# Kernel tuning notes

Measured on AMD Instinct MI355X. Metric: run time of the kernel, lower is better.

The kernel has to match this reference:

```python
import jax, jax.numpy as jnp
import numpy as np

B, C, N, K, OUT = 4, 3, 32768, 16, 64


def setup_inputs() -> dict:
    key = jax.random.key(0)
    k1, k2, k3, k4, k5, k6 = jax.random.split(key, 6)
    coords = jax.random.normal(k1, (B, C, N), dtype=jnp.float32)
    knn_indices = jax.random.randint(k2, (B, N, K), 0, N, dtype=jnp.int64)
    # Conv2d(3, 64, (1,1)) weight is (out, in, 1, 1) -> store as (out, in)
    W1 = jax.random.normal(k3, (OUT, C), dtype=jnp.float32) * (1.0 / np.sqrt(C))
    b1 = jax.random.normal(k4, (OUT,), dtype=jnp.float32) * 0.01
    W2 = jax.random.normal(k5, (OUT, OUT), dtype=jnp.float32) * (1.0 / np.sqrt(OUT))
    b2 = jax.random.normal(k6, (OUT,), dtype=jnp.float32) * 0.01
    return {"coords": coords, "knn_indices": knn_indices,
            "W1": W1, "b1": b1, "W2": W2, "b2": b2}


def reference(coords, knn_indices, W1, b1, W2, b2):
    b, c, n = coords.shape
    _, _, k = knn_indices.shape
    # index2points: gather neighbor coords -> (B, C, N, K)
    idx = knn_indices.reshape(b, 1, n * k)                      # (B,1,N*K)
    idx = jnp.broadcast_to(idx, (b, c, n * k))
    knn_coords = jnp.take_along_axis(coords, idx, axis=2).reshape(b, c, n, k)
    # localize(coords, knn_coords) * -1  ==  coords - knn_coords
    coords_space = coords[:, :, :, None] - knn_coords           # (B,C,N,K)
    # 1x1 conv MLP: conv -> relu -> conv
    h = jnp.einsum('oc,bcnk->bonk', W1, coords_space) + b1[None, :, None, None]
    h = jax.nn.relu(h)
    out = jnp.einsum('oc,bcnk->bonk', W2, h) + b2[None, :, None, None]
    return out
```

## Files before the change

kernel.cpp:

```cpp
#include <hip/hip_runtime.h>
#include <hip/hip_bf16.h>


typedef __attribute__((ext_vector_type(8))) short bf16x8;
typedef __attribute__((ext_vector_type(4))) float f32x4;

#define N_PTS 32768
#define K_NB  16
#define C_OUT 64
#define NPW   8

__device__ __forceinline__ short f2b(float x) {
    __hip_bfloat16 h = __float2bfloat16(x);
    return reinterpret_cast<short&>(h);
}

__global__ __launch_bounds__(256) void pe_kernel(
    const float* __restrict__ coords,
    const int*   __restrict__ knn,
    const float* __restrict__ W1,
    const float* __restrict__ b1,
    const float* __restrict__ W2,
    const float* __restrict__ b2,
    float*       __restrict__ out)
{
    const int lane = (int)(threadIdx.x & 63);
    const int wid  = (int)(threadIdx.x >> 6);
    const int g    = lane >> 4;
    const int q    = lane & 15;

    __shared__ float lds[4][C_OUT * 32];
    float* myl = lds[wid];

    float w1r[2][8][3], b1r[2][8];
#pragma unroll
    for (int s = 0; s < 2; ++s)
#pragma unroll
        for (int i = 0; i < 8; ++i) {
            int j = 32 * s + 8 * g + i;
            w1r[s][i][0] = W1[j * 3 + 0];
            w1r[s][i][1] = W1[j * 3 + 1];
            w1r[s][i][2] = W1[j * 3 + 2];
            b1r[s][i]    = b1[j];
        }

    bf16x8 wfrag[4][2];
#pragma unroll
    for (int mt = 0; mt < 4; ++mt)
#pragma unroll
        for (int s = 0; s < 2; ++s)
#pragma unroll
            for (int i = 0; i < 8; ++i)
                wfrag[mt][s][i] = f2b(W2[(16 * mt + q) * 64 + 32 * s + 8 * g + i]);

    float b2r[4];
#pragma unroll
    for (int mt = 0; mt < 4; ++mt)
        b2r[mt] = b2[16 * mt + q];

    const int col0 = ((int)blockIdx.x * 4 + wid) * NPW;

    for (int tp = 0; tp < NPW / 2; ++tp) {
        const int col = __builtin_amdgcn_readfirstlane(col0 + 2 * tp);
        const int b  = col >> 15;
        const int n0 = col & (N_PTS - 1);

        const int*   kb = knn + ((size_t)(b << 15) + n0) * K_NB;
        const float* cb = coords + (size_t)b * (3 * N_PTS);

        int i0 = kb[q];
        int i1 = kb[K_NB + q];

        float e0 = cb[n0];
        float e1 = cb[N_PTS + n0];
        float e2 = cb[2 * N_PTS + n0];
        float f0 = cb[n0 + 1];
        float f1 = cb[N_PTS + n0 + 1];
        float f2 = cb[2 * N_PTS + n0 + 1];

        float a0 = e0 - cb[i0];
        float a1 = e1 - cb[N_PTS + i0];
        float a2 = e2 - cb[2 * N_PTS + i0];
        float c0 = f0 - cb[i1];
        float c1 = f1 - cb[N_PTS + i1];
        float c2 = f2 - cb[2 * N_PTS + i1];

        bf16x8 h0[2], h1[2];
#pragma unroll
        for (int s = 0; s < 2; ++s)
#pragma unroll
            for (int i = 0; i < 8; ++i) {
                float u = fmaf(w1r[s][i][0], a0,
                          fmaf(w1r[s][i][1], a1,
                          fmaf(w1r[s][i][2], a2, b1r[s][i])));
                h0[s][i] = f2b(fmaxf(u, 0.0f));
                float v = fmaf(w1r[s][i][0], c0,
                          fmaf(w1r[s][i][1], c1,
                          fmaf(w1r[s][i][2], c2, b1r[s][i])));
                h1[s][i] = f2b(fmaxf(v, 0.0f));
            }

#pragma unroll
        for (int p = 0; p < 2; ++p) {
#pragma unroll
            for (int mt = 0; mt < 4; ++mt) {
                f32x4 acc = { b2r[mt], b2r[mt], b2r[mt], b2r[mt] };
#pragma unroll
                for (int s = 0; s < 2; ++s)
                    acc = __builtin_amdgcn_mfma_f32_16x16x32_bf16(
                              (p == 0 ? h0[s] : h1[s]), wfrag[mt][s], acc, 0, 0, 0);
                const int o = 16 * mt + q;
                const int chunk = (4 * p + g) ^ (q & 7);
                *(f32x4*)(myl + o * 32 + chunk * 4) = acc;
            }
        }

        const int r = lane >> 3;
        const int c = lane & 7;
        const int cs = c ^ r;
        const size_t nbase = ((size_t)(b * C_OUT) * N_PTS + n0) * K_NB + c * 4;
        const size_t ostride = (size_t)N_PTS * K_NB;
#pragma unroll
        for (int i = 0; i < 8; ++i) {
            const int o = 8 * i + r;
            f32x4 vdat = *(const f32x4*)(myl + o * 32 + cs * 4);
            __builtin_nontemporal_store(vdat,
                (f32x4*)(out + nbase + (size_t)o * ostride));
        }
    }
}

extern "C" void kernel_launch(void* const* d_in, const int* in_sizes, int n_in,
                              void* d_out, int out_size, void* d_ws, size_t ws_size,
                              hipStream_t stream) {
    const float* coords = (const float*)d_in[0];
    const int*   knn    = (const int*)d_in[1];
    const float* W1     = (const float*)d_in[2];
    const float* b1     = (const float*)d_in[3];
    const float* W2     = (const float*)d_in[4];
    const float* b2     = (const float*)d_in[5];
    float* out = (float*)d_out;

    dim3 grid(4096), block(256);
    hipLaunchKernelGGL(pe_kernel, grid, block, 0, stream,
                       coords, knn, W1, b1, W2, b2, out);
}
```

Measured before the change: 102.9 us.

## Process four points per iteration and store full 256-byte output rows

Each wave now handles four consecutive points per loop iteration instead of two, so every output channel row it writes covers 64 contiguous floats (256 bytes) rather than 128 bytes. LDS staging is reorganized into two halves of 32 output channels with a 16-way XOR swizzle, and the loop is kept rolled. The goal is wider, more coalesced nontemporal stores and more independent gathers in flight per iteration, at the cost of higher register pressure from the four hidden fragments.

Result: no change. 102.8 us (-0.1%).

```diff
diff --git a/kernel.cpp b/kernel.cpp
--- a/kernel.cpp
+++ b/kernel.cpp
@@ -29,7 +29,7 @@
     const int g    = lane >> 4;
     const int q    = lane & 15;
 
-    __shared__ float lds[4][C_OUT * 32];
+    __shared__ float lds[4][32 * 64];
     float* myl = lds[wid];
 
     float w1r[2][8][3], b1r[2][8];
@@ -60,72 +60,72 @@
 
     const int col0 = ((int)blockIdx.x * 4 + wid) * NPW;
 
-    for (int tp = 0; tp < NPW / 2; ++tp) {
-        const int col = __builtin_amdgcn_readfirstlane(col0 + 2 * tp);
+#pragma unroll 1
+    for (int tq = 0; tq < NPW / 4; ++tq) {
+        const int col = __builtin_amdgcn_readfirstlane(col0 + 4 * tq);
         const int b  = col >> 15;
         const int n0 = col & (N_PTS - 1);
 
         const int*   kb = knn + ((size_t)(b << 15) + n0) * K_NB;
         const float* cb = coords + (size_t)b * (3 * N_PTS);
 
-        int i0 = kb[q];
-        int i1 = kb[K_NB + q];
+        int idxp[4];
+#pragma unroll
+        for (int p = 0; p < 4; ++p)
+            idxp[p] = kb[K_NB * p + q];
 
-        float e0 = cb[n0];
-        float e1 = cb[N_PTS + n0];
-        float e2 = cb[2 * N_PTS + n0];
-        float f0 = cb[n0 + 1];
-        float f1 = cb[N_PTS + n0 + 1];
-        float f2 = cb[2 * N_PTS + n0 + 1];
+        float d[4][3];
+#pragma unroll
+        for (int p = 0; p < 4; ++p) {
+            d[p][0] = cb[n0 + p]             - cb[idxp[p]];
+            d[p][1] = cb[N_PTS + n0 + p]     - cb[N_PTS + idxp[p]];
+            d[p][2] = cb[2 * N_PTS + n0 + p] - cb[2 * N_PTS + idxp[p]];
+        }
 
-        float a0 = e0 - cb[i0];
-        float a1 = e1 - cb[N_PTS + i0];
-        float a2 = e2 - cb[2 * N_PTS + i0];
-        float c0 = f0 - cb[i1];
-        float c1 = f1 - cb[N_PTS + i1];
-        float c2 = f2 - cb[2 * N_PTS + i1];
+        bf16x8 hfrag[4][2];
+#pragma unroll
+        for (int p = 0; p < 4; ++p)
+#pragma unroll
+            for (int s = 0; s < 2; ++s)
+#pragma unroll
+                for (int i = 0; i < 8; ++i) {
+                    float u = fmaf(w1r[s][i][0], d[p][0],
+                              fmaf(w1r[s][i][1], d[p][1],
+                              fmaf(w1r[s][i][2], d[p][2], b1r[s][i])));
+                    hfrag[p][s][i] = f2b(fmaxf(u, 0.0f));
+                }
 
-        bf16x8 h0[2], h1[2];
+        const size_t ostride = (size_t)N_PTS * K_NB;
+        const size_t nbase = ((size_t)(b * C_OUT) * N_PTS + n0) * K_NB;
+
 #pragma unroll
-        for (int s = 0; s < 2; ++s)
+        for (int half = 0; half < 2; ++half) {
+#pragma unroll
+            for (int p = 0; p < 4; ++p)
+#pragma unroll
+                for (int mtl = 0; mtl < 2; ++mtl) {
+                    const int mt = 2 * half + mtl;
+                    f32x4 acc = { b2r[mt], b2r[mt], b2r[mt], b2r[mt] };
+#pragma unroll
+                    for (int s = 0; s < 2; ++s)
+                        acc = __builtin_amdgcn_mfma_f32_16x16x32_bf16(
+                                  hfrag[p][s], wfrag[mt][s], acc, 0, 0, 0);
+                    const int row = 16 * mtl + q;
+                    const int ch  = (4 * p + g) ^ (row & 15);
+                    *(f32x4*)(myl + row * 64 + ch * 4) = acc;
+                }
+
+            const int rin  = lane >> 4;
+            const int chm  = lane & 15;
 #pragma unroll
             for (int i = 0; i < 8; ++i) {
-                float u = fmaf(w1r[s][i][0], a0,
-                          fmaf(w1r[s][i][1], a1,
-                          fmaf(w1r[s][i][2], a2, b1r[s][i])));
-                h0[s][i] = f2b(fmaxf(u, 0.0f));
-                float v = fmaf(w1r[s][i][0], c0,
-                          fmaf(w1r[s][i][1], c1,
-                          fmaf(w1r[s][i][2], c2, b1r[s][i])));
-                h1[s][i] = f2b(fmaxf(v, 0.0f));
+                const int row = 4 * i + rin;
+                const int chl = chm ^ (row & 15);
+                f32x4 vdat = *(const f32x4*)(myl + row * 64 + chl * 4);
+                const int o = 32 * half + row;
+                __builtin_nontemporal_store(vdat,
+                    (f32x4*)(out + nbase + (size_t)o * ostride + chm * 4));
             }
-
-#pragma unroll
-        for (int p = 0; p < 2; ++p) {
-#pragma unroll
-            for (int mt = 0; mt < 4; ++mt) {
-                f32x4 acc = { b2r[mt], b2r[mt], b2r[mt], b2r[mt] };
-#pragma unroll
-                for (int s = 0; s < 2; ++s)
-                    acc = __builtin_amdgcn_mfma_f32_16x16x32_bf16(
-                              (p == 0 ? h0[s] : h1[s]), wfrag[mt][s], acc, 0, 0, 0);
-                const int o = 16 * mt + q;
-                const int chunk = (4 * p + g) ^ (q & 7);
-                *(f32x4*)(myl + o * 32 + chunk * 4) = acc;
-            }
-        }
-
-        const int r = lane >> 3;
-        const int c = lane & 7;
-        const int cs = c ^ r;
-        const size_t nbase = ((size_t)(b * C_OUT) * N_PTS + n0) * K_NB + c * 4;
-        const size_t ostride = (size_t)N_PTS * K_NB;
-#pragma unroll
-        for (int i = 0; i < 8; ++i) {
-            const int o = 8 * i + r;
-            f32x4 vdat = *(const f32x4*)(myl + o * 32 + cs * 4);
-            __builtin_nontemporal_store(vdat,
-                (f32x4*)(out + nbase + (size_t)o * ostride));
         }
     }
 }
```
